# Kernel tuning notes

Hardware: AMD Instinct MI355X
Metric: run time of the kernel (lower is better)

Reference implementation:

```python
import jax, jax.numpy as jnp
import numpy as np

EMBED_DIM = 1024
NUM_HEADS = 16
HEAD_DIM = EMBED_DIM // NUM_HEADS


def setup_inputs() -> dict:
    key = jax.random.key(0)
    ks = jax.random.split(key, 9)
    B, T, D = 2, 4096, EMBED_DIM
    scale = 1.0 / np.sqrt(D)
    x = jax.random.normal(ks[0], (B, T, D), dtype=jnp.float32)
    # nn.Linear weights stored as (out, in); we use (in, out) layout via transpose-free init
    Wq = jax.random.uniform(ks[1], (D, D), dtype=jnp.float32, minval=-scale, maxval=scale)
    Wk = jax.random.uniform(ks[2], (D, D), dtype=jnp.float32, minval=-scale, maxval=scale)
    Wv = jax.random.uniform(ks[3], (D, D), dtype=jnp.float32, minval=-scale, maxval=scale)
    Wo = jax.random.uniform(ks[4], (D, D), dtype=jnp.float32, minval=-scale, maxval=scale)
    bq = jax.random.uniform(ks[5], (D,), dtype=jnp.float32, minval=-scale, maxval=scale)
    bk = jax.random.uniform(ks[6], (D,), dtype=jnp.float32, minval=-scale, maxval=scale)
    bv = jax.random.uniform(ks[7], (D,), dtype=jnp.float32, minval=-scale, maxval=scale)
    bo = jax.random.uniform(ks[8], (D,), dtype=jnp.float32, minval=-scale, maxval=scale)
    return {"x": x, "Wq": Wq, "bq": bq, "Wk": Wk, "bk": bk,
            "Wv": Wv, "bv": bv, "Wo": Wo, "bo": bo}


def reference(x, Wq, bq, Wk, bk, Wv, bv, Wo, bo):
    B, T, D = x.shape
    H, Hd = NUM_HEADS, HEAD_DIM
    q = x @ Wq + bq  # [B,T,D]
    k = x @ Wk + bk
    v = x @ Wv + bv
    # [B,T,D] -> [B,H,T,Hd]
    q = q.reshape(B, T, H, Hd).transpose(0, 2, 1, 3)
    k = k.reshape(B, T, H, Hd).transpose(0, 2, 1, 3)
    v = v.reshape(B, T, H, Hd).transpose(0, 2, 1, 3)
    att = jnp.einsum('bhqd,bhkd->bhqk', q, k) / jnp.sqrt(jnp.float32(Hd))
    causal = jnp.tril(jnp.ones((T, T), dtype=bool))  # True = keep
    att = jnp.where(causal, att, -jnp.inf)
    att = jax.nn.softmax(att, axis=-1)
    out = jnp.einsum('bhqk,bhkd->bhqd', att, v)  # [B,H,T,Hd]
    out = out.transpose(0, 2, 1, 3).reshape(B, T, D)
    return out @ Wo + bo
```

## Files before the change

### kernel.cpp

```cpp
#include <hip/hip_runtime.h>
#include <hip/hip_bf16.h>
#include <math.h>

typedef __bf16 bf16;
typedef __attribute__((ext_vector_type(8))) __bf16 bf16x8;
typedef __attribute__((ext_vector_type(4))) __bf16 bf16x4;
typedef __attribute__((ext_vector_type(4))) short short4v;
typedef __attribute__((ext_vector_type(4))) float f32x4;

#define MFMA16(a,b,c)  __builtin_amdgcn_mfma_f32_16x16x32_bf16((a),(b),(c),0,0,0)
#define MFMAK16(a,b,c) __builtin_amdgcn_mfma_f32_16x16x16bf16_1k((a),(b),(c),0,0,0)

__device__ __forceinline__ void gload16(const void* gp, void* lp) {
  __builtin_amdgcn_global_load_lds(
      (const __attribute__((address_space(1))) void*)gp,
      (__attribute__((address_space(3))) void*)lp, 16, 0, 0);
}

__global__ __launch_bounds__(256) void cast_x(
    const float* __restrict__ x, bf16* __restrict__ xb)
{
  size_t i = ((size_t)blockIdx.x*256 + threadIdx.x) * 8;
  f32x4 a = *(const f32x4*)(x+i);
  f32x4 b = *(const f32x4*)(x+i+4);
  bf16x8 o;
  #pragma unroll
  for (int j=0;j<4;j++) { o[j] = (bf16)a[j]; o[4+j] = (bf16)b[j]; }
  *(bf16x8*)(xb+i) = o;
}

__global__ __launch_bounds__(1024) void tr_cast(
    const float* __restrict__ w0, const float* __restrict__ w1,
    const float* __restrict__ w2, bf16* __restrict__ dst)
{
  __shared__ bf16 tile[64][65];
  const float* src = (blockIdx.z==0)?w0:(blockIdx.z==1)?w1:w2;
  bf16* d = dst + (size_t)blockIdx.z * (1024*1024);
  int x = threadIdx.x, y = threadIdx.y;
  int tc = blockIdx.x, tr = blockIdx.y;
  #pragma unroll
  for (int i=0;i<4;i++) {
    int r = y + i*16;
    tile[r][x] = (bf16)src[(size_t)(tr*64+r)*1024 + tc*64 + x];
  }
  __syncthreads();
  #pragma unroll
  for (int i=0;i<4;i++) {
    int r = y + i*16;
    d[(size_t)(tc*64+r)*1024 + tr*64 + x] = tile[x][r];
  }
}

__global__ __launch_bounds__(256) void gemm_qkv(
    const bf16* __restrict__ A, const bf16* __restrict__ Bt,
    const float* __restrict__ bq, const float* __restrict__ bk, const float* __restrict__ bv,
    bf16* __restrict__ q, bf16* __restrict__ k, bf16* __restrict__ v,
    int M, int K)
{
  __shared__ __align__(16) bf16 As[128*32];
  __shared__ __align__(16) bf16 Bs[128*32];
  const int tid  = threadIdx.x;
  const int wave = tid >> 6;
  const int lane = tid & 63;
  const int l15  = lane & 15;
  const int quad = lane >> 4;
  const int m0 = blockIdx.y * 128;
  const int n0 = blockIdx.x * 128;
  const int wm = (wave >> 1) * 64;
  const int wn = (wave & 1) * 64;
  const int srow = lane >> 2;
  const int scol = (lane & 3) * 8;

  f32x4 acc[4][4];
  #pragma unroll
  for (int i=0;i<4;i++)
    #pragma unroll
    for (int j=0;j<4;j++)
      acc[i][j] = (f32x4){0.f,0.f,0.f,0.f};

  for (int k0 = 0; k0 < K; k0 += 32) {
    __syncthreads();
    #pragma unroll
    for (int p=0;p<2;p++) {
      int c = p*4 + wave;
      int row = c*16 + srow;
      gload16(A  + (size_t)(m0+row)*K + k0 + scol, As + c*512);
      gload16(Bt + (size_t)(n0+row)*K + k0 + scol, Bs + c*512);
    }
    __syncthreads();
    bf16x8 af[4], bfr[4];
    #pragma unroll
    for (int t=0;t<4;t++) {
      af[t]  = *(const bf16x8*)(As + (wm + t*16 + l15)*32 + quad*8);
      bfr[t] = *(const bf16x8*)(Bs + (wn + t*16 + l15)*32 + quad*8);
    }
    #pragma unroll
    for (int mt=0;mt<4;mt++)
      #pragma unroll
      for (int nt=0;nt<4;nt++)
        acc[mt][nt] = MFMA16(af[mt], bfr[nt], acc[mt][nt]);
  }

  const int mat = n0 >> 10;
  if (mat == 2) {
    #pragma unroll
    for (int nt=0;nt<4;nt++) {
      int col = (n0 & 1023) + wn + nt*16 + l15;
      int hh = col >> 6, dl = col & 63;
      float bvv = bv[col];
      #pragma unroll
      for (int mt=0;mt<4;mt++) {
        int row = m0 + wm + mt*16 + quad*4;
        int bb = row >> 12, tt = row & 4095;
        bf16x4 o;
        #pragma unroll
        for (int r=0;r<4;r++) o[r] = (bf16)(acc[mt][nt][r] + bvv);
        *(bf16x4*)(v + ((size_t)((bb*16 + hh)*64 + dl))*4096 + tt) = o;
      }
    }
  } else {
    const float* bsel = (mat==0) ? bq : bk;
    bf16*       osel  = (mat==0) ? q  : k;
    const float qsc   = (mat==0) ? 0.1803368801f : 1.0f;
    #pragma unroll
    for (int nt=0;nt<4;nt++) {
      int col = n0 + wn + nt*16 + l15;
      int cw  = col & 1023;
      float bvv = bsel[cw];
      #pragma unroll
      for (int mt=0;mt<4;mt++) {
        int row = m0 + wm + mt*16 + quad*4;
        #pragma unroll
        for (int r=0;r<4;r++)
          osel[(size_t)(row + r)*1024 + cw] = (bf16)((acc[mt][nt][r] + bvv) * qsc);
      }
    }
  }
}

__global__ __launch_bounds__(256) void gemm_out(
    const bf16* __restrict__ A, const bf16* __restrict__ Bt,
    const float* __restrict__ bias, float* __restrict__ C,
    int M, int N, int K)
{
  __shared__ __align__(16) bf16 As[128*32];
  __shared__ __align__(16) bf16 Bs[128*32];
  const int tid  = threadIdx.x;
  const int wave = tid >> 6;
  const int lane = tid & 63;
  const int l15  = lane & 15;
  const int quad = lane >> 4;
  const int m0 = blockIdx.y * 128;
  const int n0 = blockIdx.x * 128;
  const int wm = (wave >> 1) * 64;
  const int wn = (wave & 1) * 64;
  const int srow = lane >> 2;
  const int scol = (lane & 3) * 8;

  f32x4 acc[4][4];
  #pragma unroll
  for (int i=0;i<4;i++)
    #pragma unroll
    for (int j=0;j<4;j++)
      acc[i][j] = (f32x4){0.f,0.f,0.f,0.f};

  for (int k0 = 0; k0 < K; k0 += 32) {
    __syncthreads();
    #pragma unroll
    for (int p=0;p<2;p++) {
      int c = p*4 + wave;
      int row = c*16 + srow;
      gload16(A  + (size_t)(m0+row)*K + k0 + scol, As + c*512);
      gload16(Bt + (size_t)(n0+row)*K + k0 + scol, Bs + c*512);
    }
    __syncthreads();
    bf16x8 af[4], bfr[4];
    #pragma unroll
    for (int t=0;t<4;t++) {
      af[t]  = *(const bf16x8*)(As + (wm + t*16 + l15)*32 + quad*8);
      bfr[t] = *(const bf16x8*)(Bs + (wn + t*16 + l15)*32 + quad*8);
    }
    #pragma unroll
    for (int mt=0;mt<4;mt++)
      #pragma unroll
      for (int nt=0;nt<4;nt++)
        acc[mt][nt] = MFMA16(af[mt], bfr[nt], acc[mt][nt]);
  }

  #pragma unroll
  for (int nt=0;nt<4;nt++) {
    int col = n0 + wn + nt*16 + l15;
    float bvv = bias[col];
    #pragma unroll
    for (int mt=0;mt<4;mt++) {
      int row = m0 + wm + mt*16 + quad*4;
      #pragma unroll
      for (int r=0;r<4;r++)
        C[(size_t)(row + r)*N + col] = acc[mt][nt][r] + bvv;
    }
  }
}

__global__ __launch_bounds__(256, 5) void attn_fwd(
    const bf16* __restrict__ Q, const bf16* __restrict__ Kp,
    const bf16* __restrict__ Vt, bf16* __restrict__ O)
{
  __shared__ __align__(16) char KsB[2*8192];
  __shared__ __align__(16) char VtB[2*8192];

  const int tid  = threadIdx.x;
  const int w    = tid >> 6;
  const int lane = tid & 63;
  const int l15  = lane & 15;
  const int quad = lane >> 4;

  const int bid = blockIdx.x;
  const int qt  = 63 - (bid >> 5);
  const int bh  = bid & 31;
  const int h   = bh & 15;
  const int b   = bh >> 4;

  const size_t headoff = (size_t)h * 64;
  const size_t bbase   = (size_t)b * 4096;

  bf16x8 aq[2];
  {
    int row = qt*64 + w*16 + l15;
    const bf16* qp = Q + (bbase + row)*1024 + headoff + quad*8;
    aq[0] = *(const bf16x8*)(qp);
    aq[1] = *(const bf16x8*)(qp + 32);
  }

  short4v ones_s;
  {
    bf16x4 o1;
    #pragma unroll
    for (int j=0;j<4;j++) o1[j] = (bf16)1.0f;
    ones_s = __builtin_bit_cast(short4v, o1);
  }

  f32x4 acco[4];
  f32x4 accli;
  #pragma unroll
  for (int i=0;i<4;i++) acco[i] = (f32x4){0.f,0.f,0.f,0.f};
  accli = (f32x4){0.f,0.f,0.f,0.f};

  const int kt_row = tid >> 2;
  const int kswz   = (kt_row & 7) << 4;
  const int ks_w0  = kt_row*128 + (((tid & 3)*32)      ^ kswz);
  const int ks_w1  = kt_row*128 + (((tid & 3)*32 + 16) ^ kswz);

  const int vd  = tid >> 2;
  const int vt0 = (tid & 3) * 16;
  int vw[4];
  #pragma unroll
  for (int u=0;u<4;u++)
    vw[u] = vd*128 + (((vt0 + u*4)*2) ^ ((vd & 15) << 3));
  const bf16* vbase = Vt + ((size_t)(b*16 + h) * 64 + vd) * 4096 + vt0;

  const int s7    = l15 & 7;
  const int ks_r0 = l15*128 + ((quad ^ (s7 & 3)) << 4) + ((s7 >> 2) << 6);
  const int ks_r1 = ks_r0 ^ 64;
  const int vt_rbase = l15*128 + ((quad ^ (l15 & 3)) << 3) + ((l15 >> 2) << 5);
  int vt_r[4];
  #pragma unroll
  for (int tt=0;tt<4;tt++) vt_r[tt] = vt_rbase ^ (tt << 5);

  {
    const bf16* kp = Kp + (bbase + kt_row)*1024 + headoff + (tid & 3)*16;
    bf16x8 k0 = *(const bf16x8*)(kp);
    bf16x8 k1 = *(const bf16x8*)(kp + 8);
    *(bf16x8*)(KsB + ks_w0) = k0;
    *(bf16x8*)(KsB + ks_w1) = k1;
    bf16x8 v0 = *(const bf16x8*)(vbase);
    bf16x8 v1 = *(const bf16x8*)(vbase + 8);
    *(bf16x4*)(VtB + vw[0]) = __builtin_shufflevector(v0, v0, 0,1,2,3);
    *(bf16x4*)(VtB + vw[1]) = __builtin_shufflevector(v0, v0, 4,5,6,7);
    *(bf16x4*)(VtB + vw[2]) = __builtin_shufflevector(v1, v1, 0,1,2,3);
    *(bf16x4*)(VtB + vw[3]) = __builtin_shufflevector(v1, v1, 4,5,6,7);
  }
  __syncthreads();

  const bf16* kpref = Kp + (bbase + 64 + kt_row)*1024 + headoff + (tid & 3)*16;
  const bf16* vpref = vbase + 64;

  for (int kt = 0; kt <= qt; ++kt) {
    const int p = kt & 1;
    const bool pre = (kt < qt);

    bf16x8 kr0, kr1, vr0, vr1;
    if (pre) {
      kr0 = *(const bf16x8*)(kpref);
      kr1 = *(const bf16x8*)(kpref + 8);
      vr0 = *(const bf16x8*)(vpref);
      vr1 = *(const bf16x8*)(vpref + 8);
      kpref += 64*1024;
      vpref += 64;
    }

    const char* ksb = KsB + p*8192;
    const char* vtb = VtB + p*8192;

    f32x4 accs[4];
    #pragma unroll
    for (int i=0;i<4;i++) accs[i] = (f32x4){0.f,0.f,0.f,0.f};

    __builtin_amdgcn_s_setprio(1);
    #pragma unroll
    for (int kk=0;kk<2;kk++) {
      #pragma unroll
      for (int tt=0;tt<4;tt++) {
        bf16x8 ka = *(const bf16x8*)(ksb + (kk ? ks_r1 : ks_r0) + tt*2048);
        accs[tt] = MFMA16(ka, aq[kk], accs[tt]);
      }
    }
    __builtin_amdgcn_s_setprio(0);

    const bool diag = (kt == qt);
    short4v pts[4];
    #pragma unroll
    for (int tt=0;tt<4;tt++) {
      bf16x4 pb;
      #pragma unroll
      for (int r=0;r<4;r++) {
        float tv = fminf(accs[tt][r], 60.0f);
        float pf = __builtin_amdgcn_exp2f(tv);
        if (diag && (tt*16 + quad*4 + r > w*16 + l15)) pf = 0.0f;
        pb[r] = (bf16)pf;
      }
      pts[tt] = __builtin_bit_cast(short4v, pb);
    }

    __builtin_amdgcn_s_setprio(1);
    #pragma unroll
    for (int nt=0;nt<4;nt++) {
      #pragma unroll
      for (int tt=0;tt<4;tt++) {
        bf16x4 va = *(const bf16x4*)(vtb + vt_r[tt] + nt*2048);
        acco[nt] = MFMAK16(__builtin_bit_cast(short4v, va), pts[tt], acco[nt]);
      }
    }
    #pragma unroll
    for (int tt=0;tt<4;tt++)
      accli = MFMAK16(ones_s, pts[tt], accli);
    __builtin_amdgcn_s_setprio(0);

    if (pre) {
      char* ksn = KsB + (p^1)*8192;
      char* vtn = VtB + (p^1)*8192;
      *(bf16x8*)(ksn + ks_w0) = kr0;
      *(bf16x8*)(ksn + ks_w1) = kr1;
      *(bf16x4*)(vtn + vw[0]) = __builtin_shufflevector(vr0, vr0, 0,1,2,3);
      *(bf16x4*)(vtn + vw[1]) = __builtin_shufflevector(vr0, vr0, 4,5,6,7);
      *(bf16x4*)(vtn + vw[2]) = __builtin_shufflevector(vr1, vr1, 0,1,2,3);
      *(bf16x4*)(vtn + vw[3]) = __builtin_shufflevector(vr1, vr1, 4,5,6,7);
      __syncthreads();
    }
  }

  {
    float inv = 1.0f / accli[0];
    int qrow = qt*64 + w*16 + l15;
    bf16* ob = O + (bbase + qrow)*1024 + headoff;
    #pragma unroll
    for (int nt=0;nt<4;nt++) {
      bf16x4 o;
      #pragma unroll
      for (int r=0;r<4;r++) o[r] = (bf16)(acco[nt][r] * inv);
      *(bf16x4*)(ob + nt*16 + quad*4) = o;
    }
  }
}

extern "C" void kernel_launch(void* const* d_in, const int* in_sizes, int n_in,
                              void* d_out, int out_size, void* d_ws, size_t ws_size,
                              hipStream_t stream) {
  const float* x  = (const float*)d_in[0];
  const float* Wq = (const float*)d_in[1];
  const float* bq = (const float*)d_in[2];
  const float* Wk = (const float*)d_in[3];
  const float* bk = (const float*)d_in[4];
  const float* Wv = (const float*)d_in[5];
  const float* bv = (const float*)d_in[6];
  const float* Wo = (const float*)d_in[7];
  const float* bo = (const float*)d_in[8];
  float* out = (float*)d_out;

  bf16* ws = (bf16*)d_ws;
  bf16* q  = ws;
  bf16* k  = q + (size_t)8192*1024;
  bf16* v  = k + (size_t)8192*1024;
  bf16* xb = v + (size_t)8192*1024;
  bf16* ao = q;
  bf16* WtQKV = (bf16*)d_out;
  bf16* WtO   = xb;

  tr_cast<<<dim3(16,16,3), dim3(64,16), 0, stream>>>(Wq, Wk, Wv, WtQKV);
  cast_x<<<4096, 256, 0, stream>>>(x, xb);
  gemm_qkv<<<dim3(24,64), 256, 0, stream>>>(xb, WtQKV, bq, bk, bv, q, k, v, 8192, 1024);
  tr_cast<<<dim3(16,16,1), dim3(64,16), 0, stream>>>(Wo, Wo, Wo, WtO);
  attn_fwd<<<2048, 256, 0, stream>>>(q, k, v, ao);
  gemm_out<<<dim3(8,64), 256, 0, stream>>>(ao, WtO, bo, out, 8192, 1024, 1024);
}
```

Measured before the change: 334.7 us.

## Pair causal query tiles per block and transpose V in a separate kernel

```diff
diff --git a/kernel.cpp b/kernel.cpp
--- a/kernel.cpp
+++ b/kernel.cpp
@@ -48,6 +48,29 @@
   for (int i=0;i<4;i++) {
     int r = y + i*16;
     d[(size_t)(tc*64+r)*1024 + tr*64 + x] = tile[x][r];
+  }
+}
+
+__global__ __launch_bounds__(1024) void v_tr(
+    const bf16* __restrict__ v, bf16* __restrict__ vt)
+{
+  __shared__ bf16 tile[64][65];
+  int x = threadIdx.x, y = threadIdx.y;
+  int tt = blockIdx.x;
+  int bh = blockIdx.y;
+  int b = bh >> 4, h = bh & 15;
+  const bf16* src = v + ((size_t)b*4096 + tt*64)*1024 + h*64;
+  bf16* dst = vt + ((size_t)bh*64)*4096 + tt*64;
+  #pragma unroll
+  for (int i=0;i<4;i++) {
+    int r = y + i*16;
+    tile[r][x] = src[(size_t)r*1024 + x];
+  }
+  __syncthreads();
+  #pragma unroll
+  for (int i=0;i<4;i++) {
+    int r = y + i*16;
+    dst[(size_t)r*4096 + x] = tile[x][r];
   }
 }
 
@@ -102,38 +125,20 @@
   }
 
   const int mat = n0 >> 10;
-  if (mat == 2) {
-    #pragma unroll
-    for (int nt=0;nt<4;nt++) {
-      int col = (n0 & 1023) + wn + nt*16 + l15;
-      int hh = col >> 6, dl = col & 63;
-      float bvv = bv[col];
-      #pragma unroll
-      for (int mt=0;mt<4;mt++) {
-        int row = m0 + wm + mt*16 + quad*4;
-        int bb = row >> 12, tt = row & 4095;
-        bf16x4 o;
-        #pragma unroll
-        for (int r=0;r<4;r++) o[r] = (bf16)(acc[mt][nt][r] + bvv);
-        *(bf16x4*)(v + ((size_t)((bb*16 + hh)*64 + dl))*4096 + tt) = o;
-      }
-    }
-  } else {
-    const float* bsel = (mat==0) ? bq : bk;
-    bf16*       osel  = (mat==0) ? q  : k;
-    const float qsc   = (mat==0) ? 0.1803368801f : 1.0f;
-    #pragma unroll
-    for (int nt=0;nt<4;nt++) {
-      int col = n0 + wn + nt*16 + l15;
-      int cw  = col & 1023;
-      float bvv = bsel[cw];
-      #pragma unroll
-      for (int mt=0;mt<4;mt++) {
-        int row = m0 + wm + mt*16 + quad*4;
-        #pragma unroll
-        for (int r=0;r<4;r++)
-          osel[(size_t)(row + r)*1024 + cw] = (bf16)((acc[mt][nt][r] + bvv) * qsc);
-      }
+  const float* bsel = (mat==0) ? bq : (mat==1) ? bk : bv;
+  bf16*       osel  = (mat==0) ? q  : (mat==1) ? k  : v;
+  const float qsc   = (mat==0) ? 0.1803368801f : 1.0f;
+  #pragma unroll
+  for (int nt=0;nt<4;nt++) {
+    int col = n0 + wn + nt*16 + l15;
+    int cw  = col & 1023;
+    float bvv = bsel[cw];
+    #pragma unroll
+    for (int mt=0;mt<4;mt++) {
+      int row = m0 + wm + mt*16 + quad*4;
+      #pragma unroll
+      for (int r=0;r<4;r++)
+        osel[(size_t)(row + r)*1024 + cw] = (bf16)((acc[mt][nt][r] + bvv) * qsc);
     }
   }
 }
@@ -201,9 +206,9 @@
   }
 }
 
-__global__ __launch_bounds__(256, 5) void attn_fwd(
+__global__ __launch_bounds__(256, 4) void attn_fwd(
     const bf16* __restrict__ Q, const bf16* __restrict__ Kp,
-    const bf16* __restrict__ Vt, bf16* __restrict__ O)
+    const bf16* __restrict__ Vtg, bf16* __restrict__ O)
 {
   __shared__ __align__(16) char KsB[2*8192];
   __shared__ __align__(16) char VtB[2*8192];
@@ -215,7 +220,7 @@
   const int quad = lane >> 4;
 
   const int bid = blockIdx.x;
-  const int qt  = 63 - (bid >> 5);
+  const int pp  = bid >> 5;
   const int bh  = bid & 31;
   const int h   = bh & 15;
   const int b   = bh >> 4;
@@ -223,14 +228,6 @@
   const size_t headoff = (size_t)h * 64;
   const size_t bbase   = (size_t)b * 4096;
 
-  bf16x8 aq[2];
-  {
-    int row = qt*64 + w*16 + l15;
-    const bf16* qp = Q + (bbase + row)*1024 + headoff + quad*8;
-    aq[0] = *(const bf16x8*)(qp);
-    aq[1] = *(const bf16x8*)(qp + 32);
-  }
-
   short4v ones_s;
   {
     bf16x4 o1;
@@ -238,12 +235,6 @@
     for (int j=0;j<4;j++) o1[j] = (bf16)1.0f;
     ones_s = __builtin_bit_cast(short4v, o1);
   }
-
-  f32x4 acco[4];
-  f32x4 accli;
-  #pragma unroll
-  for (int i=0;i<4;i++) acco[i] = (f32x4){0.f,0.f,0.f,0.f};
-  accli = (f32x4){0.f,0.f,0.f,0.f};
 
   const int kt_row = tid >> 2;
   const int kswz   = (kt_row & 7) << 4;
@@ -256,7 +247,6 @@
   #pragma unroll
   for (int u=0;u<4;u++)
     vw[u] = vd*128 + (((vt0 + u*4)*2) ^ ((vd & 15) << 3));
-  const bf16* vbase = Vt + ((size_t)(b*16 + h) * 64 + vd) * 4096 + vt0;
 
   const int s7    = l15 & 7;
   const int ks_r0 = l15*128 + ((quad ^ (s7 & 3)) << 4) + ((s7 >> 2) << 6);
@@ -266,108 +256,139 @@
   #pragma unroll
   for (int tt=0;tt<4;tt++) vt_r[tt] = vt_rbase ^ (tt << 5);
 
-  {
-    const bf16* kp = Kp + (bbase + kt_row)*1024 + headoff + (tid & 3)*16;
-    bf16x8 k0 = *(const bf16x8*)(kp);
-    bf16x8 k1 = *(const bf16x8*)(kp + 8);
-    *(bf16x8*)(KsB + ks_w0) = k0;
-    *(bf16x8*)(KsB + ks_w1) = k1;
-    bf16x8 v0 = *(const bf16x8*)(vbase);
-    bf16x8 v1 = *(const bf16x8*)(vbase + 8);
-    *(bf16x4*)(VtB + vw[0]) = __builtin_shufflevector(v0, v0, 0,1,2,3);
-    *(bf16x4*)(VtB + vw[1]) = __builtin_shufflevector(v0, v0, 4,5,6,7);
-    *(bf16x4*)(VtB + vw[2]) = __builtin_shufflevector(v1, v1, 0,1,2,3);
-    *(bf16x4*)(VtB + vw[3]) = __builtin_shufflevector(v1, v1, 4,5,6,7);
-  }
-  __syncthreads();
-
-  const bf16* kpref = Kp + (bbase + 64 + kt_row)*1024 + headoff + (tid & 3)*16;
-  const bf16* vpref = vbase + 64;
-
-  for (int kt = 0; kt <= qt; ++kt) {
-    const int p = kt & 1;
-    const bool pre = (kt < qt);
-
-    bf16x8 kr0, kr1, vr0, vr1;
-    if (pre) {
-      kr0 = *(const bf16x8*)(kpref);
-      kr1 = *(const bf16x8*)(kpref + 8);
-      vr0 = *(const bf16x8*)(vpref);
-      vr1 = *(const bf16x8*)(vpref + 8);
-      kpref += 64*1024;
-      vpref += 64;
-    }
-
-    const char* ksb = KsB + p*8192;
-    const char* vtb = VtB + p*8192;
-
-    f32x4 accs[4];
-    #pragma unroll
-    for (int i=0;i<4;i++) accs[i] = (f32x4){0.f,0.f,0.f,0.f};
-
-    __builtin_amdgcn_s_setprio(1);
-    #pragma unroll
-    for (int kk=0;kk<2;kk++) {
-      #pragma unroll
-      for (int tt=0;tt<4;tt++) {
-        bf16x8 ka = *(const bf16x8*)(ksb + (kk ? ks_r1 : ks_r0) + tt*2048);
-        accs[tt] = MFMA16(ka, aq[kk], accs[tt]);
-      }
-    }
-    __builtin_amdgcn_s_setprio(0);
-
-    const bool diag = (kt == qt);
-    short4v pts[4];
-    #pragma unroll
-    for (int tt=0;tt<4;tt++) {
-      bf16x4 pb;
-      #pragma unroll
-      for (int r=0;r<4;r++) {
-        float tv = fminf(accs[tt][r], 60.0f);
-        float pf = __builtin_amdgcn_exp2f(tv);
-        if (diag && (tt*16 + quad*4 + r > w*16 + l15)) pf = 0.0f;
-        pb[r] = (bf16)pf;
-      }
-      pts[tt] = __builtin_bit_cast(short4v, pb);
-    }
-
-    __builtin_amdgcn_s_setprio(1);
-    #pragma unroll
-    for (int nt=0;nt<4;nt++) {
-      #pragma unroll
-      for (int tt=0;tt<4;tt++) {
-        bf16x4 va = *(const bf16x4*)(vtb + vt_r[tt] + nt*2048);
-        acco[nt] = MFMAK16(__builtin_bit_cast(short4v, va), pts[tt], acco[nt]);
-      }
-    }
-    #pragma unroll
-    for (int tt=0;tt<4;tt++)
-      accli = MFMAK16(ones_s, pts[tt], accli);
-    __builtin_amdgcn_s_setprio(0);
-
-    if (pre) {
-      char* ksn = KsB + (p^1)*8192;
-      char* vtn = VtB + (p^1)*8192;
-      *(bf16x8*)(ksn + ks_w0) = kr0;
-      *(bf16x8*)(ksn + ks_w1) = kr1;
-      *(bf16x4*)(vtn + vw[0]) = __builtin_shufflevector(vr0, vr0, 0,1,2,3);
-      *(bf16x4*)(vtn + vw[1]) = __builtin_shufflevector(vr0, vr0, 4,5,6,7);
-      *(bf16x4*)(vtn + vw[2]) = __builtin_shufflevector(vr1, vr1, 0,1,2,3);
-      *(bf16x4*)(vtn + vw[3]) = __builtin_shufflevector(vr1, vr1, 4,5,6,7);
-      __syncthreads();
-    }
-  }
-
-  {
-    float inv = 1.0f / accli[0];
-    int qrow = qt*64 + w*16 + l15;
-    bf16* ob = O + (bbase + qrow)*1024 + headoff;
-    #pragma unroll
-    for (int nt=0;nt<4;nt++) {
-      bf16x4 o;
-      #pragma unroll
-      for (int r=0;r<4;r++) o[r] = (bf16)(acco[nt][r] * inv);
-      *(bf16x4*)(ob + nt*16 + quad*4) = o;
+  const bf16* kbase0 = Kp  + (bbase + kt_row)*1024 + headoff + (tid & 3)*16;
+  const bf16* vbase0 = Vtg + ((size_t)(bh*64) + vd)*4096 + vt0;
+
+  for (int ph = 0; ph < 2; ++ph) {
+    const int qt = ph ? (63 - pp) : pp;
+    const int q0 = qt * 64;
+
+    bf16x8 aq[2];
+    {
+      int row = q0 + w*16 + l15;
+      const bf16* qp = Q + (bbase + row)*1024 + headoff + quad*8;
+      aq[0] = *(const bf16x8*)(qp);
+      aq[1] = *(const bf16x8*)(qp + 32);
+    }
+
+    f32x4 acco[4];
+    f32x4 accli;
+    #pragma unroll
+    for (int i=0;i<4;i++) acco[i] = (f32x4){0.f,0.f,0.f,0.f};
+    accli = (f32x4){0.f,0.f,0.f,0.f};
+
+    __syncthreads();
+    {
+      bf16x8 k0 = *(const bf16x8*)(kbase0);
+      bf16x8 k1 = *(const bf16x8*)(kbase0 + 8);
+      *(bf16x8*)(KsB + ks_w0) = k0;
+      *(bf16x8*)(KsB + ks_w1) = k1;
+      bf16x8 v0 = *(const bf16x8*)(vbase0);
+      bf16x8 v1 = *(const bf16x8*)(vbase0 + 8);
+      *(bf16x4*)(VtB + vw[0]) = __builtin_shufflevector(v0, v0, 0,1,2,3);
+      *(bf16x4*)(VtB + vw[1]) = __builtin_shufflevector(v0, v0, 4,5,6,7);
+      *(bf16x4*)(VtB + vw[2]) = __builtin_shufflevector(v1, v1, 0,1,2,3);
+      *(bf16x4*)(VtB + vw[3]) = __builtin_shufflevector(v1, v1, 4,5,6,7);
+    }
+    __syncthreads();
+
+    const bf16* kpref = kbase0 + 64*1024;
+    const bf16* vpref = vbase0 + 64;
+
+    for (int kt = 0; kt <= qt; ++kt) {
+      const int p = kt & 1;
+      const bool pre = (kt < qt);
+
+      bf16x8 kr0, kr1, vr0, vr1;
+      if (pre) {
+        kr0 = *(const bf16x8*)(kpref);
+        kr1 = *(const bf16x8*)(kpref + 8);
+        vr0 = *(const bf16x8*)(vpref);
+        vr1 = *(const bf16x8*)(vpref + 8);
+        kpref += 64*1024;
+        vpref += 64;
+      }
+
+      const char* ksb = KsB + p*8192;
+      const char* vtb = VtB + p*8192;
+
+      f32x4 accs[4];
+      #pragma unroll
+      for (int i=0;i<4;i++) accs[i] = (f32x4){0.f,0.f,0.f,0.f};
+
+      __builtin_amdgcn_s_setprio(1);
+      #pragma unroll
+      for (int kk=0;kk<2;kk++) {
+        #pragma unroll
+        for (int tt=0;tt<4;tt++) {
+          bf16x8 ka = *(const bf16x8*)(ksb + (kk ? ks_r1 : ks_r0) + tt*2048);
+          accs[tt] = MFMA16(ka, aq[kk], accs[tt]);
+        }
+      }
+      __builtin_amdgcn_s_setprio(0);
+
+      short4v pts[4];
+      if (kt == qt) {
+        #pragma unroll
+        for (int tt=0;tt<4;tt++) {
+          bf16x4 pb;
+          #pragma unroll
+          for (int r=0;r<4;r++) {
+            float pf = __builtin_amdgcn_exp2f(fminf(accs[tt][r], 60.0f));
+            if (tt*16 + quad*4 + r > w*16 + l15) pf = 0.0f;
+            pb[r] = (bf16)pf;
+          }
+          pts[tt] = __builtin_bit_cast(short4v, pb);
+        }
+      } else {
+        #pragma unroll
+        for (int tt=0;tt<4;tt++) {
+          bf16x4 pb;
+          #pragma unroll
+          for (int r=0;r<4;r++)
+            pb[r] = (bf16)__builtin_amdgcn_exp2f(fminf(accs[tt][r], 60.0f));
+          pts[tt] = __builtin_bit_cast(short4v, pb);
+        }
+      }
+
+      __builtin_amdgcn_s_setprio(1);
+      #pragma unroll
+      for (int nt=0;nt<4;nt++) {
+        #pragma unroll
+        for (int tt=0;tt<4;tt++) {
+          bf16x4 va = *(const bf16x4*)(vtb + vt_r[tt] + nt*2048);
+          acco[nt] = MFMAK16(__builtin_bit_cast(short4v, va), pts[tt], acco[nt]);
+        }
+      }
+      #pragma unroll
+      for (int tt=0;tt<4;tt++)
+        accli = MFMAK16(ones_s, pts[tt], accli);
+      __builtin_amdgcn_s_setprio(0);
+
+      if (pre) {
+        char* ksn = KsB + (p^1)*8192;
+        char* vtn = VtB + (p^1)*8192;
+        *(bf16x8*)(ksn + ks_w0) = kr0;
+        *(bf16x8*)(ksn + ks_w1) = kr1;
+        *(bf16x4*)(vtn + vw[0]) = __builtin_shufflevector(vr0, vr0, 0,1,2,3);
+        *(bf16x4*)(vtn + vw[1]) = __builtin_shufflevector(vr0, vr0, 4,5,6,7);
+        *(bf16x4*)(vtn + vw[2]) = __builtin_shufflevector(vr1, vr1, 0,1,2,3);
+        *(bf16x4*)(vtn + vw[3]) = __builtin_shufflevector(vr1, vr1, 4,5,6,7);
+        __syncthreads();
+      }
+    }
+
+    {
+      float inv = 1.0f / accli[0];
+      int qrow = q0 + w*16 + l15;
+      bf16* ob = O + (bbase + qrow)*1024 + headoff;
+      #pragma unroll
+      for (int nt=0;nt<4;nt++) {
+        bf16x4 o;
+        #pragma unroll
+        for (int r=0;r<4;r++) o[r] = (bf16)(acco[nt][r] * inv);
+        *(bf16x4*)(ob + nt*16 + quad*4) = o;
+      }
     }
   }
 }
@@ -393,12 +414,14 @@
   bf16* xb = v + (size_t)8192*1024;
   bf16* ao = q;
   bf16* WtQKV = (bf16*)d_out;
+  bf16* vT    = (bf16*)d_out;
   bf16* WtO   = xb;
 
   tr_cast<<<dim3(16,16,3), dim3(64,16), 0, stream>>>(Wq, Wk, Wv, WtQKV);
   cast_x<<<4096, 256, 0, stream>>>(x, xb);
   gemm_qkv<<<dim3(24,64), 256, 0, stream>>>(xb, WtQKV, bq, bk, bv, q, k, v, 8192, 1024);
+  v_tr<<<dim3(64,32), dim3(64,16), 0, stream>>>(v, vT);
   tr_cast<<<dim3(16,16,1), dim3(64,16), 0, stream>>>(Wo, Wo, Wo, WtO);
-  attn_fwd<<<2048, 256, 0, stream>>>(q, k, v, ao);
+  attn_fwd<<<1024, 256, 0, stream>>>(q, k, vT, ao);
   gemm_out<<<dim3(8,64), 256, 0, stream>>>(ao, WtO, bo, out, 8192, 1024, 1024);
 }
```

Measured after the change: 329.2 us. About the same (-1.6%).
